# Performance work log

Measured on AMD Instinct MI355X. Metric: run time of the kernel, lower is better.

## Reference

```python
import jax, jax.numpy as jnp
import numpy as np

N_NODES = 100000
N_EDGES = 1600000
N_GRAPHS = 1000
X_S = 128
HID = 64


def setup_inputs() -> dict:
    key = jax.random.key(0)
    ks = jax.random.split(key, 12)
    x = jax.random.normal(ks[0], (N_NODES, X_S), dtype=jnp.float32)
    edge_index = jax.random.randint(ks[1], (2, N_EDGES), 0, N_NODES, dtype=jnp.int64)
    batch = jnp.sort(jax.random.randint(ks[2], (N_NODES,), 0, N_GRAPHS, dtype=jnp.int64))
    def lin(k, fin, fout):
        s = 1.0 / np.sqrt(fin)
        kw, kb = jax.random.split(k)
        W = jax.random.uniform(kw, (fin, fout), minval=-s, maxval=s, dtype=jnp.float32)
        b = jax.random.uniform(kb, (fout,), minval=-s, maxval=s, dtype=jnp.float32)
        return W, b
    W1, b1 = lin(ks[3], X_S, HID)
    W2, b2 = lin(ks[4], HID, HID)
    W3, b3 = lin(ks[5], HID, HID)
    Wf, bf = lin(ks[6], HID, 10)
    Wl, bl = lin(ks[7], 10, 1)
    eps1 = jnp.float32(0.37)
    eps2 = jnp.float32(0.72)
    eps3 = jnp.float32(0.11)
    return {"x": x, "edge_index": edge_index, "batch": batch,
            "W1": W1, "b1": b1, "W2": W2, "b2": b2, "W3": W3, "b3": b3,
            "Wf": Wf, "bf": bf, "Wl": Wl, "bl": bl,
            "eps1": eps1, "eps2": eps2, "eps3": eps3}


def _gin_conv(h, src, dst, eps, W, b):
    # GIN: nn((1+eps)*x_i + sum_{j in N(i)} x_j); messages flow src -> dst
    agg = jax.ops.segment_sum(h[src], dst, num_segments=N_NODES)  # [N, d]
    return ((1.0 + eps) * h + agg) @ W + b


def reference(x, edge_index, batch, W1, b1, W2, b2, W3, b3, Wf, bf, Wl, bl,
              eps1, eps2, eps3):
    src, dst = edge_index[0], edge_index[1]
    h = jax.nn.relu(_gin_conv(x, src, dst, eps1, W1, b1))
    h = jax.nn.relu(_gin_conv(h, src, dst, eps2, W2, b2))
    h = jax.nn.relu(_gin_conv(h, src, dst, eps3, W3, b3))
    # global_mean_pool over graph ids
    sums = jax.ops.segment_sum(h, batch, num_segments=N_GRAPHS)        # [G, 64]
    cnts = jax.ops.segment_sum(jnp.ones((N_NODES,), h.dtype), batch,
                               num_segments=N_GRAPHS)                   # [G]
    pooled = sums / jnp.maximum(cnts, 1.0)[:, None]
    out = jax.nn.relu(pooled @ Wf + bf) @ Wl + bl                       # [G, 1]
    return out
```

## Files before the change

kernel.cpp:

```cpp
#include <hip/hip_runtime.h>

#define N_NODES 100000
#define N_EDGES 1600000
#define N_GRAPHS 1000

#define NB_C 782
#define B1   256
#define CHUNK (N_EDGES / B1)
#define MTOT (NB_C * B1)

#define LSTR 68

typedef unsigned int uint32;
typedef unsigned short ushort16;

static __device__ __forceinline__ ushort16 f2bf(float f) {
    uint32 u = __float_as_uint(f);
    u += 0x7fffu + ((u >> 16) & 1u);
    return (ushort16)(u >> 16);
}
static __device__ __forceinline__ uint32 pk2(float a, float b) {
    return (uint32)f2bf(a) | ((uint32)f2bf(b) << 16);
}
static __device__ __forceinline__ void bf2x(uint32 v, float& lo, float& hi) {
    lo = __uint_as_float(v << 16);
    hi = __uint_as_float(v & 0xffff0000u);
}


__global__ __launch_bounds__(256) void count_kernel(
    const int* __restrict__ dst, int* __restrict__ M)
{
    __shared__ int cnt[NB_C];
    int b = blockIdx.x, t = threadIdx.x;
    for (int q = t; q < NB_C; q += 256) cnt[q] = 0;
    __syncthreads();
    int e0 = b * CHUNK;
    for (int e = e0 + t; e < e0 + CHUNK; e += 256)
        atomicAdd(&cnt[dst[e] >> 7], 1);
    __syncthreads();
    for (int q = t; q < NB_C; q += 256) M[q * B1 + b] = cnt[q];
}

#define SCAN_B 1024
#define SCAN_NBLK ((MTOT + SCAN_B - 1) / SCAN_B)

__global__ __launch_bounds__(256) void scanA_kernel(
    const int* __restrict__ in, int* __restrict__ excl, int* __restrict__ bsum)
{
    __shared__ int s[256];
    int b = blockIdx.x, t = threadIdx.x;
    int base = b * SCAN_B + t * 4;
    int v[4];
#pragma unroll
    for (int i = 0; i < 4; ++i) v[i] = (base + i < MTOT) ? in[base + i] : 0;
    int tsum = v[0] + v[1] + v[2] + v[3];
    s[t] = tsum;
    __syncthreads();
    for (int off = 1; off < 256; off <<= 1) {
        int x = (t >= off) ? s[t - off] : 0;
        __syncthreads();
        s[t] += x;
        __syncthreads();
    }
    int run = s[t] - tsum;
#pragma unroll
    for (int i = 0; i < 4; ++i) {
        if (base + i < MTOT) excl[base + i] = run;
        run += v[i];
    }
    if (t == 255) bsum[b] = s[255];
}

__global__ __launch_bounds__(256) void scanB_kernel(int* __restrict__ bsum)
{
    __shared__ int s[256];
    int t = threadIdx.x;
    int v = (t < SCAN_NBLK) ? bsum[t] : 0;
    s[t] = v;
    __syncthreads();
    for (int off = 1; off < 256; off <<= 1) {
        int x = (t >= off) ? s[t - off] : 0;
        __syncthreads();
        s[t] += x;
        __syncthreads();
    }
    if (t < SCAN_NBLK) bsum[t] = s[t] - v;
}

__global__ __launch_bounds__(256) void scanC_kernel(
    const int* __restrict__ excl, const int* __restrict__ bsum,
    int* __restrict__ out)
{
    int b = blockIdx.x, t = threadIdx.x;
    int add = bsum[b];
    int base = b * SCAN_B + t * 4;
#pragma unroll
    for (int i = 0; i < 4; ++i)
        if (base + i < MTOT) out[base + i] = excl[base + i] + add;
}

__global__ __launch_bounds__(256) void scatter_kernel(
    const int* __restrict__ src, const int* __restrict__ dst,
    const int* __restrict__ Ms, uint32* __restrict__ tmp)
{
    __shared__ int cur[NB_C];
    int b = blockIdx.x, t = threadIdx.x;
    for (int q = t; q < NB_C; q += 256) cur[q] = Ms[q * B1 + b];
    __syncthreads();
    int e0 = b * CHUNK;
    for (int e = e0 + t; e < e0 + CHUNK; e += 256) {
        int d = dst[e];
        int q = d >> 7;
        int pos = atomicAdd(&cur[q], 1);
        tmp[pos] = ((uint32)(d & 127) << 17) | (uint32)src[e];
    }
}

__global__ __launch_bounds__(256) void finalize_kernel(
    const uint32* __restrict__ tmp, const int* __restrict__ Ms,
    int* __restrict__ row_off, int* __restrict__ esrc)
{
    __shared__ int cnt[128];
    __shared__ int pref[128];
    __shared__ int cur[128];
    int q = blockIdx.x, t = threadIdx.x;
    int start = Ms[q * B1];
    int end = (q == NB_C - 1) ? N_EDGES : Ms[(q + 1) * B1];

    if (t < 128) cnt[t] = 0;
    __syncthreads();
    for (int e = start + t; e < end; e += 256)
        atomicAdd(&cnt[tmp[e] >> 17], 1);
    __syncthreads();
    if (t < 128) pref[t] = cnt[t];
    __syncthreads();
    for (int off = 1; off < 128; off <<= 1) {
        int x = 0;
        if (t < 128 && t >= off) x = pref[t - off];
        __syncthreads();
        if (t < 128) pref[t] += x;
        __syncthreads();
    }
    if (t < 128) {
        int excl = pref[t] - cnt[t];
        int node = q * 128 + t;
        if (node < N_NODES) row_off[node] = start + excl;
        cur[t] = start + excl;
    }
    if (q == 0 && t == 0) row_off[N_NODES] = N_EDGES;
    __syncthreads();
    for (int e = start + t; e < end; e += 256) {
        uint32 u = tmp[e];
        int pos = atomicAdd(&cur[u >> 17], 1);
        esrc[pos] = (int)(u & 0x1FFFFu);
    }
}

template<int IN>
__global__ __launch_bounds__(256) void gemm_kernel(
    const float* __restrict__ h,
    const float* __restrict__ W,
    ushort16* __restrict__ y)
{
    __shared__ float hs[64 * LSTR];
    __shared__ float wsh[64 * 64];

    const int t = threadIdx.x;
    const int node0 = blockIdx.x * 64;
    const int m = t >> 4;
    const int p = t & 15;

    float4 acc[4];
#pragma unroll
    for (int i = 0; i < 4; ++i) acc[i] = make_float4(0.f, 0.f, 0.f, 0.f);

    for (int kb = 0; kb < IN / 64; ++kb) {
        if (kb) __syncthreads();
        {
            int kc = (t & 15) * 4;
            int rbase = t >> 4;
#pragma unroll
            for (int rr = 0; rr < 4; ++rr) {
                int row = rr * 16 + rbase;
                int node = node0 + row;
                float4 v = make_float4(0.f, 0.f, 0.f, 0.f);
                if (node < N_NODES)
                    v = *(const float4*)&h[(size_t)node * IN + kb * 64 + kc];
                *(float4*)&hs[row * LSTR + kc] = v;
            }
        }
        {
            int j4 = (t & 15) * 4;
            int kbase = t >> 4;
#pragma unroll
            for (int it = 0; it < 4; ++it) {
                int k = it * 16 + kbase;
                *(float4*)&wsh[k * 64 + j4] =
                    *(const float4*)&W[(size_t)(kb * 64 + k) * 64 + j4];
            }
        }
        __syncthreads();

        const float* hb = &hs[(m * 4) * LSTR];
#pragma unroll 4
        for (int kc = 0; kc < 64; kc += 4) {
            float4 hv[4];
#pragma unroll
            for (int i = 0; i < 4; ++i) hv[i] = *(const float4*)&hb[i * LSTR + kc];
            float4 w0 = *(const float4*)&wsh[(kc + 0) * 64 + p * 4];
            float4 w1 = *(const float4*)&wsh[(kc + 1) * 64 + p * 4];
            float4 w2 = *(const float4*)&wsh[(kc + 2) * 64 + p * 4];
            float4 w3 = *(const float4*)&wsh[(kc + 3) * 64 + p * 4];
#pragma unroll
            for (int i = 0; i < 4; ++i) {
                acc[i].x = fmaf(hv[i].x, w0.x, acc[i].x);
                acc[i].y = fmaf(hv[i].x, w0.y, acc[i].y);
                acc[i].z = fmaf(hv[i].x, w0.z, acc[i].z);
                acc[i].w = fmaf(hv[i].x, w0.w, acc[i].w);
                acc[i].x = fmaf(hv[i].y, w1.x, acc[i].x);
                acc[i].y = fmaf(hv[i].y, w1.y, acc[i].y);
                acc[i].z = fmaf(hv[i].y, w1.z, acc[i].z);
                acc[i].w = fmaf(hv[i].y, w1.w, acc[i].w);
                acc[i].x = fmaf(hv[i].z, w2.x, acc[i].x);
                acc[i].y = fmaf(hv[i].z, w2.y, acc[i].y);
                acc[i].z = fmaf(hv[i].z, w2.z, acc[i].z);
                acc[i].w = fmaf(hv[i].z, w2.w, acc[i].w);
                acc[i].x = fmaf(hv[i].w, w3.x, acc[i].x);
                acc[i].y = fmaf(hv[i].w, w3.y, acc[i].y);
                acc[i].z = fmaf(hv[i].w, w3.z, acc[i].z);
                acc[i].w = fmaf(hv[i].w, w3.w, acc[i].w);
            }
        }
    }

#pragma unroll
    for (int i = 0; i < 4; ++i) {
        int node = node0 + m * 4 + i;
        if (node >= N_NODES) continue;
        *(uint2*)&y[(size_t)node * 64 + p * 4] =
            make_uint2(pk2(acc[i].x, acc[i].y), pk2(acc[i].z, acc[i].w));
    }
}

__global__ __launch_bounds__(256) void gemm_bf16_kernel(
    const uint32* __restrict__ hb,
    const float* __restrict__ W,
    ushort16* __restrict__ y)
{
    __shared__ float hs[64 * LSTR];
    __shared__ float wsh[64 * 64];

    const int t = threadIdx.x;
    const int node0 = blockIdx.x * 64;

    {
        int w = t & 7;
        int rbase = t >> 3;
#pragma unroll
        for (int rr = 0; rr < 2; ++rr) {
            int row = rr * 32 + rbase;
            int node = node0 + row;
            uint4 v = make_uint4(0u, 0u, 0u, 0u);
            if (node < N_NODES)
                v = *(const uint4*)&hb[(size_t)node * 32 + w * 4];
            float f[8];
            bf2x(v.x, f[0], f[1]);
            bf2x(v.y, f[2], f[3]);
            bf2x(v.z, f[4], f[5]);
            bf2x(v.w, f[6], f[7]);
            float* o = &hs[row * LSTR + w * 8];
            *(float4*)o       = make_float4(f[0], f[1], f[2], f[3]);
            *(float4*)(o + 4) = make_float4(f[4], f[5], f[6], f[7]);
        }
    }
    {
        int j4 = (t & 15) * 4;
        int kbase = t >> 4;
#pragma unroll
        for (int it = 0; it < 4; ++it) {
            int k = it * 16 + kbase;
            *(float4*)&wsh[k * 64 + j4] = *(const float4*)&W[(size_t)k * 64 + j4];
        }
    }
    __syncthreads();

    const int m = t >> 4;
    const int p = t & 15;
    float4 acc[4];
#pragma unroll
    for (int i = 0; i < 4; ++i) acc[i] = make_float4(0.f, 0.f, 0.f, 0.f);

    const float* hbp = &hs[(m * 4) * LSTR];
#pragma unroll 4
    for (int kc = 0; kc < 64; kc += 4) {
        float4 hv[4];
#pragma unroll
        for (int i = 0; i < 4; ++i) hv[i] = *(const float4*)&hbp[i * LSTR + kc];
        float4 w0 = *(const float4*)&wsh[(kc + 0) * 64 + p * 4];
        float4 w1 = *(const float4*)&wsh[(kc + 1) * 64 + p * 4];
        float4 w2 = *(const float4*)&wsh[(kc + 2) * 64 + p * 4];
        float4 w3 = *(const float4*)&wsh[(kc + 3) * 64 + p * 4];
#pragma unroll
        for (int i = 0; i < 4; ++i) {
            acc[i].x = fmaf(hv[i].x, w0.x, acc[i].x);
            acc[i].y = fmaf(hv[i].x, w0.y, acc[i].y);
            acc[i].z = fmaf(hv[i].x, w0.z, acc[i].z);
            acc[i].w = fmaf(hv[i].x, w0.w, acc[i].w);
            acc[i].x = fmaf(hv[i].y, w1.x, acc[i].x);
            acc[i].y = fmaf(hv[i].y, w1.y, acc[i].y);
            acc[i].z = fmaf(hv[i].y, w1.z, acc[i].z);
            acc[i].w = fmaf(hv[i].y, w1.w, acc[i].w);
            acc[i].x = fmaf(hv[i].z, w2.x, acc[i].x);
            acc[i].y = fmaf(hv[i].z, w2.y, acc[i].y);
            acc[i].z = fmaf(hv[i].z, w2.z, acc[i].z);
            acc[i].w = fmaf(hv[i].z, w2.w, acc[i].w);
            acc[i].x = fmaf(hv[i].w, w3.x, acc[i].x);
            acc[i].y = fmaf(hv[i].w, w3.y, acc[i].y);
            acc[i].z = fmaf(hv[i].w, w3.z, acc[i].z);
            acc[i].w = fmaf(hv[i].w, w3.w, acc[i].w);
        }
    }

#pragma unroll
    for (int i = 0; i < 4; ++i) {
        int node = node0 + m * 4 + i;
        if (node >= N_NODES) continue;
        *(uint2*)&y[(size_t)node * 64 + p * 4] =
            make_uint2(pk2(acc[i].x, acc[i].y), pk2(acc[i].z, acc[i].w));
    }
}

__global__ __launch_bounds__(256) void aggregate_kernel(
    const uint32* __restrict__ y,
    const int* __restrict__ row_off,
    const int* __restrict__ esrc,
    const float* __restrict__ b,
    const float* __restrict__ eps_p,
    uint32* __restrict__ outb)
{
    int lane = threadIdx.x & 63;
    int wave = threadIdx.x >> 6;
    int g = lane >> 4;
    int j = (lane >> 3) & 1;
    int w = lane & 7;
    int node = blockIdx.x * 16 + wave * 4 + g;

    int s0 = row_off[node], s1 = row_off[node + 1];
    float a[8], c[8];
#pragma unroll
    for (int i = 0; i < 8; ++i) { a[i] = 0.f; c[i] = 0.f; }

    const uint32* yw = y + (size_t)w * 4;
    int e = s0 + j;
    for (; e + 2 < s1; e += 4) {
        int i0 = esrc[e];
        int i1 = esrc[e + 2];
        uint4 v0 = *(const uint4*)&yw[(size_t)i0 * 32];
        uint4 v1 = *(const uint4*)&yw[(size_t)i1 * 32];
        float lo, hi;
        bf2x(v0.x, lo, hi); a[0] += lo; a[1] += hi;
        bf2x(v0.y, lo, hi); a[2] += lo; a[3] += hi;
        bf2x(v0.z, lo, hi); a[4] += lo; a[5] += hi;
        bf2x(v0.w, lo, hi); a[6] += lo; a[7] += hi;
        bf2x(v1.x, lo, hi); c[0] += lo; c[1] += hi;
        bf2x(v1.y, lo, hi); c[2] += lo; c[3] += hi;
        bf2x(v1.z, lo, hi); c[4] += lo; c[5] += hi;
        bf2x(v1.w, lo, hi); c[6] += lo; c[7] += hi;
    }
    if (e < s1) {
        int i0 = esrc[e];
        uint4 v0 = *(const uint4*)&yw[(size_t)i0 * 32];
        float lo, hi;
        bf2x(v0.x, lo, hi); a[0] += lo; a[1] += hi;
        bf2x(v0.y, lo, hi); a[2] += lo; a[3] += hi;
        bf2x(v0.z, lo, hi); a[4] += lo; a[5] += hi;
        bf2x(v0.w, lo, hi); a[6] += lo; a[7] += hi;
    }
#pragma unroll
    for (int i = 0; i < 8; ++i) {
        a[i] += c[i];
        a[i] += __shfl_xor(a[i], 8);
    }

    if (j == 0) {
        uint4 sv = *(const uint4*)&yw[(size_t)node * 32];
        float s[8];
        bf2x(sv.x, s[0], s[1]);
        bf2x(sv.y, s[2], s[3]);
        bf2x(sv.z, s[4], s[5]);
        bf2x(sv.w, s[6], s[7]);
        float ep1 = 1.0f + eps_p[0];
        float4 b0 = *(const float4*)&b[w * 8];
        float4 b1 = *(const float4*)&b[w * 8 + 4];
        float r0 = fmaxf(fmaf(ep1, s[0], a[0]) + b0.x, 0.0f);
        float r1 = fmaxf(fmaf(ep1, s[1], a[1]) + b0.y, 0.0f);
        float r2 = fmaxf(fmaf(ep1, s[2], a[2]) + b0.z, 0.0f);
        float r3 = fmaxf(fmaf(ep1, s[3], a[3]) + b0.w, 0.0f);
        float r4 = fmaxf(fmaf(ep1, s[4], a[4]) + b1.x, 0.0f);
        float r5 = fmaxf(fmaf(ep1, s[5], a[5]) + b1.y, 0.0f);
        float r6 = fmaxf(fmaf(ep1, s[6], a[6]) + b1.z, 0.0f);
        float r7 = fmaxf(fmaf(ep1, s[7], a[7]) + b1.w, 0.0f);
        *(uint4*)&outb[(size_t)node * 32 + w * 4] =
            make_uint4(pk2(r0, r1), pk2(r2, r3), pk2(r4, r5), pk2(r6, r7));
    }
}

__global__ __launch_bounds__(256) void pool_head_kernel(
    const uint32* __restrict__ hb,
    const int* __restrict__ batch,
    const float* __restrict__ Wf,
    const float* __restrict__ bfv,
    const float* __restrict__ Wl,
    const float* __restrict__ blv,
    float* __restrict__ out)
{
    __shared__ float red[4][64];
    __shared__ float pooled[64];
    __shared__ float hid[10];
    int g = blockIdx.x;
    int t = threadIdx.x;
    int lo = 0, hi = N_NODES;
    while (lo < hi) { int mid = (lo + hi) >> 1; if (batch[mid] < g) lo = mid + 1; else hi = mid; }
    int start = lo;
    hi = N_NODES;
    while (lo < hi) { int mid = (lo + hi) >> 1; if (batch[mid] < g + 1) lo = mid + 1; else hi = mid; }
    int end = lo;

    int c = t & 63, nl = t >> 6;
    int wd = c >> 1, odd = c & 1;
    float acc = 0.0f;
    for (int i = start + nl; i < end; i += 4) {
        uint32 u = hb[(size_t)i * 32 + wd];
        acc += __uint_as_float(odd ? (u & 0xffff0000u) : (u << 16));
    }
    red[nl][c] = acc;
    __syncthreads();
    if (t < 64) {
        float cnt = (float)(end - start);
        float inv = 1.0f / fmaxf(cnt, 1.0f);
        pooled[t] = (red[0][t] + red[1][t] + red[2][t] + red[3][t]) * inv;
    }
    __syncthreads();
    if (t < 10) {
        float s = bfv[t];
#pragma unroll
        for (int k = 0; k < 64; ++k) s = fmaf(pooled[k], Wf[k * 10 + t], s);
        hid[t] = fmaxf(s, 0.0f);
    }
    __syncthreads();
    if (t == 0) {
        float s = blv[0];
#pragma unroll
        for (int j = 0; j < 10; ++j) s = fmaf(hid[j], Wl[j], s);
        out[g] = s;
    }
}

extern "C" void kernel_launch(void* const* d_in, const int* in_sizes, int n_in,
                              void* d_out, int out_size, void* d_ws, size_t ws_size,
                              hipStream_t stream)
{
    const float* x     = (const float*)d_in[0];
    const int*   ei    = (const int*)  d_in[1];
    const int*   src   = ei;
    const int*   dst   = ei + N_EDGES;
    const int*   batch = (const int*)  d_in[2];
    const float* W1    = (const float*)d_in[3];
    const float* b1    = (const float*)d_in[4];
    const float* W2    = (const float*)d_in[5];
    const float* b2    = (const float*)d_in[6];
    const float* W3    = (const float*)d_in[7];
    const float* b3    = (const float*)d_in[8];
    const float* Wf    = (const float*)d_in[9];
    const float* bfv   = (const float*)d_in[10];
    const float* Wl    = (const float*)d_in[11];
    const float* blv   = (const float*)d_in[12];
    const float* eps1  = (const float*)d_in[13];
    const float* eps2  = (const float*)d_in[14];
    const float* eps3  = (const float*)d_in[15];

    ushort16* ybA = (ushort16*)d_ws;
    ushort16* ybB = ybA + (size_t)N_NODES * 64;
    int*   ints = (int*)(ybB + (size_t)N_NODES * 64);
    int*   M       = ints;
    int*   Mex     = M + MTOT;
    int*   Ms      = Mex + MTOT;
    int*   bsum    = Ms + MTOT;
    int*   row_off = bsum + 256;
    int*   esrc    = row_off + N_NODES + 1;
    uint32* tmp    = (uint32*)(esrc + N_EDGES);

    count_kernel<<<B1, 256, 0, stream>>>(dst, M);
    scanA_kernel<<<SCAN_NBLK, 256, 0, stream>>>(M, Mex, bsum);
    scanB_kernel<<<1, 256, 0, stream>>>(bsum);
    scanC_kernel<<<SCAN_NBLK, 256, 0, stream>>>(Mex, bsum, Ms);
    scatter_kernel<<<B1, 256, 0, stream>>>(src, dst, Ms, tmp);
    finalize_kernel<<<NB_C, 256, 0, stream>>>(tmp, Ms, row_off, esrc);

    const int gemm_blk = (N_NODES + 63) / 64;
    const int agg_blk  = N_NODES / 16;

    gemm_kernel<128><<<gemm_blk, 256, 0, stream>>>(x, W1, ybA);
    aggregate_kernel<<<agg_blk, 256, 0, stream>>>(
        (const uint32*)ybA, row_off, esrc, b1, eps1, (uint32*)ybB);

    gemm_bf16_kernel<<<gemm_blk, 256, 0, stream>>>((const uint32*)ybB, W2, ybA);
    aggregate_kernel<<<agg_blk, 256, 0, stream>>>(
        (const uint32*)ybA, row_off, esrc, b2, eps2, (uint32*)ybB);

    gemm_bf16_kernel<<<gemm_blk, 256, 0, stream>>>((const uint32*)ybB, W3, ybA);
    aggregate_kernel<<<agg_blk, 256, 0, stream>>>(
        (const uint32*)ybA, row_off, esrc, b3, eps3, (uint32*)ybB);

    pool_head_kernel<<<N_GRAPHS, 256, 0, stream>>>(
        (const uint32*)ybB, batch, Wf, bfv, Wl, blv, (float*)d_out);
}
```

Measured before the change: 342.6 us.

## Merge layer-1 GEMM with edge counting and fuse scan phases B and C

The first-layer GEMM and the per-chunk destination counting now run in one launch, with extra blocks past the GEMM grid doing the count work in shared memory. This lets the two independent stages overlap on the GPU. The second and third scan kernels are fused: each block redoes the small block-sum scan itself instead of using a separate single-block launch. Together these remove two launches and serial gaps, at the cost of a larger shared allocation for the counting blocks and repeated block-sum scans.

```diff
diff --git a/kernel.cpp b/kernel.cpp
--- a/kernel.cpp
+++ b/kernel.cpp
@@ -10,6 +10,7 @@
 #define MTOT (NB_C * B1)
 
 #define LSTR 68
+#define GEMM_BLK ((N_NODES + 63) / 64)
 
 typedef unsigned int uint32;
 typedef unsigned short ushort16;
@@ -27,146 +28,32 @@
     hi = __uint_as_float(v & 0xffff0000u);
 }
 
-
-__global__ __launch_bounds__(256) void count_kernel(
-    const int* __restrict__ dst, int* __restrict__ M)
-{
-    __shared__ int cnt[NB_C];
-    int b = blockIdx.x, t = threadIdx.x;
-    for (int q = t; q < NB_C; q += 256) cnt[q] = 0;
-    __syncthreads();
-    int e0 = b * CHUNK;
-    for (int e = e0 + t; e < e0 + CHUNK; e += 256)
-        atomicAdd(&cnt[dst[e] >> 7], 1);
-    __syncthreads();
-    for (int q = t; q < NB_C; q += 256) M[q * B1 + b] = cnt[q];
-}
-
-#define SCAN_B 1024
-#define SCAN_NBLK ((MTOT + SCAN_B - 1) / SCAN_B)
-
-__global__ __launch_bounds__(256) void scanA_kernel(
-    const int* __restrict__ in, int* __restrict__ excl, int* __restrict__ bsum)
-{
-    __shared__ int s[256];
-    int b = blockIdx.x, t = threadIdx.x;
-    int base = b * SCAN_B + t * 4;
-    int v[4];
-#pragma unroll
-    for (int i = 0; i < 4; ++i) v[i] = (base + i < MTOT) ? in[base + i] : 0;
-    int tsum = v[0] + v[1] + v[2] + v[3];
-    s[t] = tsum;
-    __syncthreads();
-    for (int off = 1; off < 256; off <<= 1) {
-        int x = (t >= off) ? s[t - off] : 0;
-        __syncthreads();
-        s[t] += x;
-        __syncthreads();
-    }
-    int run = s[t] - tsum;
-#pragma unroll
-    for (int i = 0; i < 4; ++i) {
-        if (base + i < MTOT) excl[base + i] = run;
-        run += v[i];
-    }
-    if (t == 255) bsum[b] = s[255];
-}
-
-__global__ __launch_bounds__(256) void scanB_kernel(int* __restrict__ bsum)
-{
-    __shared__ int s[256];
-    int t = threadIdx.x;
-    int v = (t < SCAN_NBLK) ? bsum[t] : 0;
-    s[t] = v;
-    __syncthreads();
-    for (int off = 1; off < 256; off <<= 1) {
-        int x = (t >= off) ? s[t - off] : 0;
-        __syncthreads();
-        s[t] += x;
-        __syncthreads();
-    }
-    if (t < SCAN_NBLK) bsum[t] = s[t] - v;
-}
-
-__global__ __launch_bounds__(256) void scanC_kernel(
-    const int* __restrict__ excl, const int* __restrict__ bsum,
-    int* __restrict__ out)
-{
-    int b = blockIdx.x, t = threadIdx.x;
-    int add = bsum[b];
-    int base = b * SCAN_B + t * 4;
-#pragma unroll
-    for (int i = 0; i < 4; ++i)
-        if (base + i < MTOT) out[base + i] = excl[base + i] + add;
-}
-
-__global__ __launch_bounds__(256) void scatter_kernel(
-    const int* __restrict__ src, const int* __restrict__ dst,
-    const int* __restrict__ Ms, uint32* __restrict__ tmp)
-{
-    __shared__ int cur[NB_C];
-    int b = blockIdx.x, t = threadIdx.x;
-    for (int q = t; q < NB_C; q += 256) cur[q] = Ms[q * B1 + b];
-    __syncthreads();
-    int e0 = b * CHUNK;
-    for (int e = e0 + t; e < e0 + CHUNK; e += 256) {
-        int d = dst[e];
-        int q = d >> 7;
-        int pos = atomicAdd(&cur[q], 1);
-        tmp[pos] = ((uint32)(d & 127) << 17) | (uint32)src[e];
-    }
-}
-
-__global__ __launch_bounds__(256) void finalize_kernel(
-    const uint32* __restrict__ tmp, const int* __restrict__ Ms,
-    int* __restrict__ row_off, int* __restrict__ esrc)
-{
-    __shared__ int cnt[128];
-    __shared__ int pref[128];
-    __shared__ int cur[128];
-    int q = blockIdx.x, t = threadIdx.x;
-    int start = Ms[q * B1];
-    int end = (q == NB_C - 1) ? N_EDGES : Ms[(q + 1) * B1];
-
-    if (t < 128) cnt[t] = 0;
-    __syncthreads();
-    for (int e = start + t; e < end; e += 256)
-        atomicAdd(&cnt[tmp[e] >> 17], 1);
-    __syncthreads();
-    if (t < 128) pref[t] = cnt[t];
-    __syncthreads();
-    for (int off = 1; off < 128; off <<= 1) {
-        int x = 0;
-        if (t < 128 && t >= off) x = pref[t - off];
-        __syncthreads();
-        if (t < 128) pref[t] += x;
-        __syncthreads();
-    }
-    if (t < 128) {
-        int excl = pref[t] - cnt[t];
-        int node = q * 128 + t;
-        if (node < N_NODES) row_off[node] = start + excl;
-        cur[t] = start + excl;
-    }
-    if (q == 0 && t == 0) row_off[N_NODES] = N_EDGES;
-    __syncthreads();
-    for (int e = start + t; e < end; e += 256) {
-        uint32 u = tmp[e];
-        int pos = atomicAdd(&cur[u >> 17], 1);
-        esrc[pos] = (int)(u & 0x1FFFFu);
-    }
-}
-
-template<int IN>
-__global__ __launch_bounds__(256) void gemm_kernel(
+__global__ __launch_bounds__(256) void gemm1_count_kernel(
     const float* __restrict__ h,
     const float* __restrict__ W,
-    ushort16* __restrict__ y)
-{
-    __shared__ float hs[64 * LSTR];
-    __shared__ float wsh[64 * 64];
-
+    ushort16* __restrict__ y,
+    const int* __restrict__ dst,
+    int* __restrict__ M)
+{
+    __shared__ __align__(16) char smem[64 * LSTR * 4 + 64 * 64 * 4];
     const int t = threadIdx.x;
+
+    if (blockIdx.x >= GEMM_BLK) {
+        int* cnt = (int*)smem;
+        int b = blockIdx.x - GEMM_BLK;
+        for (int q = t; q < NB_C; q += 256) cnt[q] = 0;
+        __syncthreads();
+        int e0 = b * CHUNK;
+        for (int e = e0 + t; e < e0 + CHUNK; e += 256)
+            atomicAdd(&cnt[dst[e] >> 7], 1);
+        __syncthreads();
+        for (int q = t; q < NB_C; q += 256) M[q * B1 + b] = cnt[q];
+        return;
+    }
+
+    float* hs  = (float*)smem;
+    float* wsh = (float*)(smem + 64 * LSTR * 4);
+
     const int node0 = blockIdx.x * 64;
     const int m = t >> 4;
     const int p = t & 15;
@@ -175,7 +62,7 @@
 #pragma unroll
     for (int i = 0; i < 4; ++i) acc[i] = make_float4(0.f, 0.f, 0.f, 0.f);
 
-    for (int kb = 0; kb < IN / 64; ++kb) {
+    for (int kb = 0; kb < 2; ++kb) {
         if (kb) __syncthreads();
         {
             int kc = (t & 15) * 4;
@@ -186,7 +73,7 @@
                 int node = node0 + row;
                 float4 v = make_float4(0.f, 0.f, 0.f, 0.f);
                 if (node < N_NODES)
-                    v = *(const float4*)&h[(size_t)node * IN + kb * 64 + kc];
+                    v = *(const float4*)&h[(size_t)node * 128 + kb * 64 + kc];
                 *(float4*)&hs[row * LSTR + kc] = v;
             }
         }
@@ -240,6 +127,115 @@
         if (node >= N_NODES) continue;
         *(uint2*)&y[(size_t)node * 64 + p * 4] =
             make_uint2(pk2(acc[i].x, acc[i].y), pk2(acc[i].z, acc[i].w));
+    }
+}
+
+#define SCAN_B 1024
+#define SCAN_NBLK ((MTOT + SCAN_B - 1) / SCAN_B)
+
+__global__ __launch_bounds__(256) void scanA_kernel(
+    const int* __restrict__ in, int* __restrict__ excl, int* __restrict__ bsum)
+{
+    __shared__ int s[256];
+    int b = blockIdx.x, t = threadIdx.x;
+    int base = b * SCAN_B + t * 4;
+    int v[4];
+#pragma unroll
+    for (int i = 0; i < 4; ++i) v[i] = (base + i < MTOT) ? in[base + i] : 0;
+    int tsum = v[0] + v[1] + v[2] + v[3];
+    s[t] = tsum;
+    __syncthreads();
+    for (int off = 1; off < 256; off <<= 1) {
+        int x = (t >= off) ? s[t - off] : 0;
+        __syncthreads();
+        s[t] += x;
+        __syncthreads();
+    }
+    int run = s[t] - tsum;
+#pragma unroll
+    for (int i = 0; i < 4; ++i) {
+        if (base + i < MTOT) excl[base + i] = run;
+        run += v[i];
+    }
+    if (t == 255) bsum[b] = s[255];
+}
+
+__global__ __launch_bounds__(256) void scanBC_kernel(
+    const int* __restrict__ excl, const int* __restrict__ bsum,
+    int* __restrict__ out)
+{
+    __shared__ int s[256];
+    int b = blockIdx.x, t = threadIdx.x;
+    int v = (t < SCAN_NBLK) ? bsum[t] : 0;
+    s[t] = v;
+    __syncthreads();
+    for (int off = 1; off < 256; off <<= 1) {
+        int x = (t >= off) ? s[t - off] : 0;
+        __syncthreads();
+        s[t] += x;
+        __syncthreads();
+    }
+    int add = s[b] - bsum[b];
+    int base = b * SCAN_B + t * 4;
+#pragma unroll
+    for (int i = 0; i < 4; ++i)
+        if (base + i < MTOT) out[base + i] = excl[base + i] + add;
+}
+
+__global__ __launch_bounds__(256) void scatter_kernel(
+    const int* __restrict__ src, const int* __restrict__ dst,
+    const int* __restrict__ Ms, uint32* __restrict__ tmp)
+{
+    __shared__ int cur[NB_C];
+    int b = blockIdx.x, t = threadIdx.x;
+    for (int q = t; q < NB_C; q += 256) cur[q] = Ms[q * B1 + b];
+    __syncthreads();
+    int e0 = b * CHUNK;
+    for (int e = e0 + t; e < e0 + CHUNK; e += 256) {
+        int d = dst[e];
+        int q = d >> 7;
+        int pos = atomicAdd(&cur[q], 1);
+        tmp[pos] = ((uint32)(d & 127) << 17) | (uint32)src[e];
+    }
+}
+
+__global__ __launch_bounds__(256) void finalize_kernel(
+    const uint32* __restrict__ tmp, const int* __restrict__ Ms,
+    int* __restrict__ row_off, int* __restrict__ esrc)
+{
+    __shared__ int cnt[128];
+    __shared__ int pref[128];
+    __shared__ int cur[128];
+    int q = blockIdx.x, t = threadIdx.x;
+    int start = Ms[q * B1];
+    int end = (q == NB_C - 1) ? N_EDGES : Ms[(q + 1) * B1];
+
+    if (t < 128) cnt[t] = 0;
+    __syncthreads();
+    for (int e = start + t; e < end; e += 256)
+        atomicAdd(&cnt[tmp[e] >> 17], 1);
+    __syncthreads();
+    if (t < 128) pref[t] = cnt[t];
+    __syncthreads();
+    for (int off = 1; off < 128; off <<= 1) {
+        int x = 0;
+        if (t < 128 && t >= off) x = pref[t - off];
+        __syncthreads();
+        if (t < 128) pref[t] += x;
+        __syncthreads();
+    }
+    if (t < 128) {
+        int excl = pref[t] - cnt[t];
+        int node = q * 128 + t;
+        if (node < N_NODES) row_off[node] = start + excl;
+        cur[t] = start + excl;
+    }
+    if (q == 0 && t == 0) row_off[N_NODES] = N_EDGES;
+    __syncthreads();
+    for (int e = start + t; e < end; e += 256) {
+        uint32 u = tmp[e];
+        int pos = atomicAdd(&cur[u >> 17], 1);
+        esrc[pos] = (int)(u & 0x1FFFFu);
     }
 }
 
@@ -491,25 +487,23 @@
     int*   esrc    = row_off + N_NODES + 1;
     uint32* tmp    = (uint32*)(esrc + N_EDGES);
 
-    count_kernel<<<B1, 256, 0, stream>>>(dst, M);
+    const int agg_blk = N_NODES / 16;
+
+    gemm1_count_kernel<<<GEMM_BLK + B1, 256, 0, stream>>>(x, W1, ybA, dst, M);
+
     scanA_kernel<<<SCAN_NBLK, 256, 0, stream>>>(M, Mex, bsum);
-    scanB_kernel<<<1, 256, 0, stream>>>(bsum);
-    scanC_kernel<<<SCAN_NBLK, 256, 0, stream>>>(Mex, bsum, Ms);
+    scanBC_kernel<<<SCAN_NBLK, 256, 0, stream>>>(Mex, bsum, Ms);
     scatter_kernel<<<B1, 256, 0, stream>>>(src, dst, Ms, tmp);
     finalize_kernel<<<NB_C, 256, 0, stream>>>(tmp, Ms, row_off, esrc);
 
-    const int gemm_blk = (N_NODES + 63) / 64;
-    const int agg_blk  = N_NODES / 16;
-
-    gemm_kernel<128><<<gemm_blk, 256, 0, stream>>>(x, W1, ybA);
     aggregate_kernel<<<agg_blk, 256, 0, stream>>>(
         (const uint32*)ybA, row_off, esrc, b1, eps1, (uint32*)ybB);
 
-    gemm_bf16_kernel<<<gemm_blk, 256, 0, stream>>>((const uint32*)ybB, W2, ybA);
+    gemm_bf16_kernel<<<GEMM_BLK, 256, 0, stream>>>((const uint32*)ybB, W2, ybA);
     aggregate_kernel<<<agg_blk, 256, 0, stream>>>(
         (const uint32*)ybA, row_off, esrc, b2, eps2, (uint32*)ybB);
 
-    gemm_bf16_kernel<<<gemm_blk, 256, 0, stream>>>((const uint32*)ybB, W3, ybA);
+    gemm_bf16_kernel<<<GEMM_BLK, 256, 0, stream>>>((const uint32*)ybB, W3, ybA);
     aggregate_kernel<<<agg_blk, 256, 0, stream>>>(
         (const uint32*)ybA, row_off, esrc, b3, eps3, (uint32*)ybB);
 
```

Result: slower. 356.2 us (+4.0%).
